# Performance work log

Hardware: AMD Instinct MI355X
Metric: run time of the kernel (lower is better)

Reference implementation:

```python
import jax, jax.numpy as jnp
import numpy as np

P = 8        # patch size
STRIDE = 4   # reference patch stride
SR = 12      # search radius
SS = 3       # search step -> 9x9 = 81 candidates
K = 16       # group size (3rd dim of 3D transform)
LAM = 2.7    # hard threshold multiplier
TWO_STEP = True


def _dct_mat(n):
    k = np.arange(n)[:, None].astype(np.float64)
    i = np.arange(n)[None, :].astype(np.float64)
    m = np.cos(np.pi * (2 * i + 1) * k / (2 * n)) * np.sqrt(2.0 / n)
    m[0] /= np.sqrt(2.0)
    return jnp.asarray(m, jnp.float32)


def _hadamard(n):
    h = np.array([[1.0]])
    while h.shape[0] < n:
        h = np.kron(h, np.array([[1.0, 1.0], [1.0, -1.0]])) / np.sqrt(2.0)
    return jnp.asarray(h, jnp.float32)

D8 = _dct_mat(P)
H16 = _hadamard(K)


def _extract_patches(img):
    # img (H, W) -> (Hp*Wp, P*P) patches at stride 1
    H, W = img.shape
    Hp, Wp = H - P + 1, W - P + 1
    cols = [img[di:di + Hp, dj:dj + Wp] for di in range(P) for dj in range(P)]
    return jnp.stack(cols, -1).reshape(Hp * Wp, P * P), Hp, Wp


def _block_match(patches, Hp, Wp):
    # returns (N, K) flat patch indices of best-matching groups
    ri = jnp.arange(0, Hp, STRIDE)
    rj = jnp.arange(0, Wp, STRIDE)
    RI, RJ = jnp.meshgrid(ri, rj, indexing='ij')
    RI, RJ = RI.reshape(-1), RJ.reshape(-1)                     # (N,)
    offs = jnp.arange(-SR, SR + 1, SS)
    OI, OJ = jnp.meshgrid(offs, offs, indexing='ij')
    ci = jnp.clip(RI[:, None] + OI.reshape(-1)[None, :], 0, Hp - 1)
    cj = jnp.clip(RJ[:, None] + OJ.reshape(-1)[None, :], 0, Wp - 1)
    cidx = ci * Wp + cj                                         # (N, C)
    cand = patches[cidx]                                        # (N, C, 64)
    ref = patches[RI * Wp + RJ]                                 # (N, 64)
    dist = (jnp.sum(cand * cand, -1)
            - 2.0 * jnp.einsum('nce,ne->nc', cand, ref)
            + jnp.sum(ref * ref, -1)[:, None])
    _, top = jax.lax.top_k(-dist, K)
    return jnp.take_along_axis(cidx, top, axis=1)               # (N, K)


def _fwd3d(groups):
    # (N, K, P*P) -> 3D transform coeffs (N, K, P, P)
    g = groups.reshape(groups.shape[0], K, P, P)
    c = jnp.einsum('ab,nkbc,dc->nkad', D8, g, D8)   # 2D DCT per patch
    return jnp.einsum('gk,nkad->ngad', H16, c)      # 1D Hadamard across group


def _inv3d(coef):
    c = jnp.einsum('gk,ngad->nkad', H16, coef)      # H^T (orthonormal)
    g = jnp.einsum('ab,nkad,dc->nkbc', D8, c, D8)   # inverse 2D DCT
    return g.reshape(coef.shape[0], K, P * P)


def _aggregate(vals, w, gidx, Hp, Wp, H, W):
    # vals (N,K,64) filtered patches, w (N,) group weights, gidx (N,K)
    gi, gj = gidx // Wp, gidx % Wp
    offs = (jnp.arange(P)[:, None] * W + jnp.arange(P)[None, :]).reshape(-1)
    pix = ((gi * W + gj)[..., None] + offs).reshape(-1)         # (N*K*64,)
    wv = jnp.broadcast_to(w[:, None, None], vals.shape)
    num = jnp.zeros(H * W, jnp.float32).at[pix].add((wv * vals).reshape(-1))
    den = jnp.zeros(H * W, jnp.float32).at[pix].add(wv.reshape(-1))
    return (num / jnp.maximum(den, 1e-8)).reshape(H, W)


def _bm3d_channel(img, sigma2):
    H, W = img.shape
    sigma2 = jnp.float32(sigma2)
    sigma = jnp.sqrt(sigma2)
    patches, Hp, Wp = _extract_patches(img)

    # ---- step 1: hard-threshold collaborative filtering ----
    gidx = _block_match(patches, Hp, Wp)
    groups = patches[gidx]                                      # (N,K,64)
    coef = _fwd3d(groups)
    mask = (jnp.abs(coef) > LAM * sigma)
    mask = mask.at[:, 0, 0, 0].set(True)                        # keep DC
    coef_ht = jnp.where(mask, coef, 0.0)
    nnz = jnp.sum(mask.astype(jnp.float32), axis=(1, 2, 3))
    w_ht = 1.0 / (sigma2 * jnp.maximum(nnz, 1.0))
    basic = _aggregate(_inv3d(coef_ht), w_ht, gidx, Hp, Wp, H, W)
    if not TWO_STEP:
        return basic

    # ---- step 2: Wiener filtering using the basic estimate ----
    patches_b, _, _ = _extract_patches(basic)
    gidx2 = _block_match(patches_b, Hp, Wp)
    cb = _fwd3d(patches_b[gidx2])                               # basic coeffs
    cn = _fwd3d(patches[gidx2])                                 # noisy coeffs
    wien = cb * cb / (cb * cb + sigma2)
    coef_w = wien * cn
    w_wie = 1.0 / (sigma2 * jnp.maximum(jnp.sum(wien * wien, axis=(1, 2, 3)), 1e-8))
    return _aggregate(_inv3d(coef_w), w_wie, gidx2, Hp, Wp, H, W)


def setup_inputs() -> dict:
    key = jax.random.key(0)
    im = jax.random.randint(key, (1, 1, 384, 384), 0, 256, dtype=jnp.int32)
    return {"im": im, "variance": 25}


def reference(im, variance):
    # im: (1, 1, H, W) int tensor, values >= 0; variance: scalar noise variance
    outs = [_bm3d_channel(im[0, c].astype(jnp.float32), variance)
            for c in range(im.shape[1])]
    return jnp.stack(outs, 0)[None]                             # (1, C, H, W) float32
```

## Files before the change

kernel.cpp:

```cpp
#include <hip/hip_runtime.h>
#include <math.h>

#define TS 45
#define FINF 3.4e38f

__device__ __forceinline__ int iclip(int v, int hi) {
  return v < 0 ? 0 : (v > hi ? hi : v);
}

constexpr float CA = 0.35355339059327373f;
constexpr float K1 = 0.49039264020161522f;
constexpr float K2 = 0.46193976625564337f;
constexpr float K3 = 0.41573480615127262f;
constexpr float K4 = 0.35355339059327379f;
constexpr float K5 = 0.27778511650980111f;
constexpr float K6 = 0.19134171618254489f;
constexpr float K7 = 0.097545161008064135f;

constexpr float DCT8[8][8] = {
  { CA, CA, CA, CA, CA, CA, CA, CA},
  { K1, K3, K5, K7,-K7,-K5,-K3,-K1},
  { K2, K6,-K6,-K2,-K2,-K6, K6, K2},
  { K3,-K7,-K1,-K5, K5, K1, K7,-K3},
  { K4,-K4,-K4, K4, K4,-K4,-K4, K4},
  { K5,-K1, K7, K3,-K3,-K7, K1,-K5},
  { K6,-K2, K2,-K6,-K6, K2,-K2, K6},
  { K7,-K5, K3,-K1, K1,-K3, K5,-K7},
};

__device__ __forceinline__ int sxor_i(int v, int m) {
  switch (m) {
    case 1:  return __builtin_amdgcn_update_dpp(0, v, 0xB1, 0xF, 0xF, true);
    case 2:  return __builtin_amdgcn_update_dpp(0, v, 0x4E, 0xF, 0xF, true);
    case 4:  return __builtin_amdgcn_ds_swizzle(v, (4 << 10) | 0x1F);
    case 8:  return __builtin_amdgcn_ds_swizzle(v, (8 << 10) | 0x1F);
    case 16: return __builtin_amdgcn_ds_swizzle(v, (16 << 10) | 0x1F);
    default: return __shfl_xor(v, 32, 64);
  }
}
__device__ __forceinline__ float sxor_f(float v, int m) {
  return __int_as_float(sxor_i(__float_as_int(v), m));
}

__device__ __forceinline__ float qbcast(float v, int s) {
  int x = __float_as_int(v), r;
  switch (s) {
    case 0:  r = __builtin_amdgcn_update_dpp(0, x, 0x00, 0xF, 0xF, true); break;
    case 1:  r = __builtin_amdgcn_update_dpp(0, x, 0x55, 0xF, 0xF, true); break;
    case 2:  r = __builtin_amdgcn_update_dpp(0, x, 0xAA, 0xF, 0xF, true); break;
    default: r = __builtin_amdgcn_update_dpp(0, x, 0xFF, 0xF, 0xF, true); break;
  }
  return __int_as_float(r);
}

__device__ __forceinline__ void fwd_rowcol(float X[2][8], float U[2][8],
                                           const float Ca0[8], const float Ca1[8]) {
#pragma unroll
  for (int r = 0; r < 2; r++)
#pragma unroll
    for (int d = 0; d < 8; d++) {
      float s = X[r][0] * DCT8[d][0];
#pragma unroll
      for (int c = 1; c < 8; c++) s += X[r][c] * DCT8[d][c];
      U[r][d] = s;
    }
#pragma unroll
  for (int r = 0; r < 2; r++)
#pragma unroll
    for (int d = 0; d < 8; d++) X[r][d] = 0.f;
#pragma unroll
  for (int b = 0; b < 8; b++)
#pragma unroll
    for (int d = 0; d < 8; d++) {
      float yb = qbcast(U[b & 1][d], b >> 1);
      X[0][d] += Ca0[b] * yb;
      X[1][d] += Ca1[b] * yb;
    }
}

__device__ __forceinline__ void inv_colrow(float X[2][8], float U[2][8],
                                           const float Ct0[8], const float Ct1[8]) {
#pragma unroll
  for (int r = 0; r < 2; r++)
#pragma unroll
    for (int d = 0; d < 8; d++) U[r][d] = 0.f;
#pragma unroll
  for (int a = 0; a < 8; a++)
#pragma unroll
    for (int d = 0; d < 8; d++) {
      float za = qbcast(X[a & 1][d], a >> 1);
      U[0][d] += Ct0[a] * za;
      U[1][d] += Ct1[a] * za;
    }
#pragma unroll
  for (int r = 0; r < 2; r++)
#pragma unroll
    for (int c = 0; c < 8; c++) {
      float s = U[r][0] * DCT8[0][c];
#pragma unroll
      for (int d = 1; d < 8; d++) s += U[r][d] * DCT8[d][c];
      X[r][c] = s;
    }
}

__device__ __forceinline__ void had16r(float X[2][8], int lane) {
#pragma unroll
  for (int m = 4; m <= 32; m <<= 1) {
    bool hi = (lane & m) != 0;
#pragma unroll
    for (int r = 0; r < 2; r++)
#pragma unroll
      for (int d = 0; d < 8; d++) {
        float tv = sxor_f(X[r][d], m);
        X[r][d] = hi ? (tv - X[r][d]) : (X[r][d] + tv);
      }
  }
#pragma unroll
  for (int r = 0; r < 2; r++)
#pragma unroll
    for (int d = 0; d < 8; d++) X[r][d] *= 0.25f;
}

template <int WIEN>
__device__ __forceinline__ void group_worker(
    const float* __restrict__ tileS, const float* __restrict__ tileN,
    float* __restrict__ accN, float* __restrict__ accD,
    const float* __restrict__ ldsD, int* __restrict__ sel,
    float* __restrict__ wdrow,
    int lane, int ri, int rj, int bi, int ub, float sigma2) {

  int cB = lane < 17 ? 64 + lane : 80;
  int aiA = iclip(ri + (lane / 9) * 3 - 12, 376) - bi;
  int ajA = iclip(rj + (lane % 9) * 3 - 12, 376) - ub;
  int aiB = iclip(ri + (cB / 9) * 3 - 12, 376) - bi;
  int ajB = iclip(rj + (cB % 9) * 3 - 12, 376) - ub;
  int roi = ri - bi, roj = rj - ub;
  float sccA = 0.f, scrA = 0.f, sccB = 0.f, scrB = 0.f, srr = 0.f;
#pragma unroll
  for (int i = 0; i < 8; i++) {
    const float* rr = tileS + (roi + i) * TS + roj;
    const float* ar = tileS + (aiA + i) * TS + ajA;
    const float* br = tileS + (aiB + i) * TS + ajB;
#pragma unroll
    for (int j = 0; j < 8; j++) {
      float rv = rr[j], av = ar[j], bv = br[j];
      sccA += av * av; scrA += av * rv;
      sccB += bv * bv; scrB += bv * rv;
      srr  += rv * rv;
    }
  }
  float d0 = sccA - 2.f * scrA + srr;
  float d1 = lane < 17 ? (sccB - 2.f * scrB + srr) : FINF;

  wdrow[lane] = d0;
  if (lane < 17)      wdrow[64 + lane] = d1;
  else if (lane < 20) wdrow[64 + lane] = FINF;

  int rank0 = 0, rank1 = 0;
  const float4* wp = (const float4*)wdrow;
  int idxB = 64 + lane;
#pragma unroll 3
  for (int c4 = 0; c4 < 21; c4++) {
    float4 v = wp[c4];
    float ev[4] = {v.x, v.y, v.z, v.w};
#pragma unroll
    for (int u = 0; u < 4; u++) {
      int c2 = c4 * 4 + u;
      rank0 += (ev[u] < d0 || (ev[u] == d0 && c2 < lane)) ? 1 : 0;
      rank1 += (ev[u] < d1 || (ev[u] == d1 && c2 < idxB)) ? 1 : 0;
    }
  }
  if (rank0 < 16) sel[rank0] = (aiA << 8) | ajA;
  if (lane < 17 && rank1 < 16) sel[rank1] = (aiB << 8) | ajB;

  int q = lane & 3, k = lane >> 2;
  float Ca0[8], Ca1[8];
#pragma unroll
  for (int b = 0; b < 8; b++) {
    Ca0[b] = ldsD[(2 * q) * 8 + b];
    Ca1[b] = ldsD[(2 * q + 1) * 8 + b];
  }
  int sp = sel[k];
  int gi = (sp >> 8) + 2 * q, gj = sp & 255;

  float X[2][8], U[2][8], ZB[2][8];
  float w;

  if (WIEN) {
#pragma unroll
    for (int r = 0; r < 2; r++)
#pragma unroll
      for (int c = 0; c < 8; c++) ZB[r][c] = tileS[(gi + r) * TS + gj + c];
    fwd_rowcol(ZB, U, Ca0, Ca1);
    had16r(ZB, lane);
  }

#pragma unroll
  for (int r = 0; r < 2; r++)
#pragma unroll
    for (int c = 0; c < 8; c++) X[r][c] = tileN[(gi + r) * TS + gj + c];
  fwd_rowcol(X, U, Ca0, Ca1);
  had16r(X, lane);

  if (WIEN) {
    float part = 0.f;
#pragma unroll
    for (int r = 0; r < 2; r++)
#pragma unroll
      for (int d = 0; d < 8; d++) {
        float cb = ZB[r][d];
        float we = cb * cb / (cb * cb + sigma2);
        X[r][d] = we * X[r][d];
        part += we * we;
      }
#pragma unroll
    for (int m = 1; m <= 32; m <<= 1) part += sxor_f(part, m);
    w = 1.f / (sigma2 * fmaxf(part, 1e-8f));
  } else {
    float thr = 2.7f * sqrtf(sigma2);
    int cnt = 0;
#pragma unroll
    for (int r = 0; r < 2; r++)
#pragma unroll
      for (int d = 0; d < 8; d++) {
        bool keep = (fabsf(X[r][d]) > thr) || (lane == 0 && r == 0 && d == 0);
        cnt += (int)__popcll(__ballot(keep));
        if (!keep) X[r][d] = 0.f;
      }
    w = 1.f / (sigma2 * fmaxf((float)cnt, 1.f));
  }

  had16r(X, lane);
#pragma unroll
  for (int a = 0; a < 8; a++) {
    Ca0[a] = ldsD[a * 8 + 2 * q];
    Ca1[a] = ldsD[a * 8 + 2 * q + 1];
  }
  inv_colrow(X, U, Ca0, Ca1);

#pragma unroll
  for (int r = 0; r < 2; r++)
#pragma unroll
    for (int c = 0; c < 8; c++) {
      int off = (gi + r) * TS + gj + c;
      atomicAdd(&accN[off], w * X[r][c]);
      atomicAdd(&accD[off], w);
    }
}

template <int WIEN>
__global__ __launch_bounds__(256, 6) void bm3d_pass(
    const int* __restrict__ img,
    const float* __restrict__ bn, const float* __restrict__ bd,
    const int* __restrict__ pvar,
    float* __restrict__ num, float* __restrict__ den) {
  __shared__ float ldsD[64];
  __shared__ int   ldsSel[4][16];
  __shared__ __align__(16) float wdist[4][84];
  __shared__ float tileN[32 * TS];
  __shared__ float tileB[WIEN ? 32 * TS : 1];
  __shared__ float accN[32 * TS], accD[32 * TS];

  int t = threadIdx.x;
  int brow = blockIdx.x / 24, bcb = blockIdx.x - brow * 24;
  int ri = brow * 4;
  int bim = ri - 12;      int bi = bim < 0 ? 0 : (bim > 352 ? 352 : bim);
  int ubm = 16 * bcb - 12; int ub = ubm < 0 ? 0 : (ubm > 352 ? 352 : ubm);

  if (t < 64) ldsD[t] = DCT8[t >> 3][t & 7];
  for (int e = t; e < 32 * 44; e += 256) {
    int r = e / 44, c = e - r * 44;
    int col = ub + c;
    bool ok = col < 384;
    int gidx = (bi + r) * 384 + col;
    tileN[r * TS + c] = ok ? (float)img[gidx] : 0.f;
    if (WIEN)
      tileB[r * TS + c] = ok ? (bn[gidx] / fmaxf(bd[gidx], 1e-8f)) : 0.f;
  }
  for (int e = t; e < 32 * TS; e += 256) { accN[e] = 0.f; accD[e] = 0.f; }
  __syncthreads();

  float sigma2 = (float)pvar[0];
  int wv = t >> 6, lane = t & 63;
  int gc = bcb * 4 + wv;
  if (gc < 95) {
    group_worker<WIEN>(WIEN ? tileB : tileN, tileN, accN, accD, ldsD,
                       &ldsSel[wv][0], &wdist[wv][0],
                       lane, ri, gc * 4, bi, ub, sigma2);
  }
  __syncthreads();

  for (int e = t; e < 32 * TS; e += 256) {
    float dv = accD[e];
    if (dv != 0.f) {
      int r = e / TS, c = e - r * TS;
      int gp = (bi + r) * 384 + ub + c;
      atomicAdd(&num[gp], accN[e]);
      atomicAdd(&den[gp], dv);
    }
  }
}

__global__ void div_kernel(const float* __restrict__ num,
                           const float* __restrict__ den,
                           float* __restrict__ out, int npix) {
  int i = blockIdx.x * blockDim.x + threadIdx.x;
  if (i < npix) out[i] = num[i] / fmaxf(den[i], 1e-8f);
}

extern "C" void kernel_launch(void* const* d_in, const int* in_sizes, int n_in,
                              void* d_out, int out_size, void* d_ws, size_t ws_size,
                              hipStream_t stream) {
  const int* img  = (const int*)d_in[0];
  const int* pvar = (const int*)d_in[1];
  float* out = (float*)d_out;
  float* ws  = (float*)d_ws;

  const int NPIX = 384 * 384;
  float* num1 = ws + 0 * NPIX;
  float* den1 = ws + 1 * NPIX;
  float* num2 = ws + 2 * NPIX;
  float* den2 = ws + 3 * NPIX;

  hipMemsetAsync(num1, 0, (size_t)4 * NPIX * sizeof(float), stream);

  const int NBLK = 95 * 24;
  bm3d_pass<0><<<NBLK, 256, 0, stream>>>(img, nullptr, nullptr, pvar, num1, den1);
  bm3d_pass<1><<<NBLK, 256, 0, stream>>>(img, num1, den1, pvar, num2, den2);
  div_kernel<<<(NPIX + 255) / 256, 256, 0, stream>>>(num2, den2, out, NPIX);
}
```

Before: 273.3 us.

## Replace global atomic aggregation with per-block slabs and a gather reduction

Each block now writes its local numerator and denominator tile to a private slab in workspace, where it previously did global atomicAdds. A separate reduce kernel gathers every overlapping block tile for each pixel and divides, producing the basic estimate and the final output. This removes the memset and the atomic contention, and folds the division for the basic estimate into the reduction. In exchange it writes about 26 MB of slab data per pass and needs enough workspace; otherwise it falls back to the atomic path.

```diff
diff --git a/kernel.cpp b/kernel.cpp
--- a/kernel.cpp
+++ b/kernel.cpp
@@ -3,6 +3,9 @@
 
 #define TS 45
 #define FINF 3.4e38f
+#define NPIX (384 * 384)
+#define NBLK (95 * 24)
+#define TILEPX (32 * 44)
 
 __device__ __forceinline__ int iclip(int v, int hi) {
   return v < 0 ? 0 : (v > hi ? hi : v);
@@ -248,7 +251,7 @@
     }
 }
 
-template <int WIEN>
+template <int WIEN, int SLAB>
 __global__ __launch_bounds__(256, 6) void bm3d_pass(
     const int* __restrict__ img,
     const float* __restrict__ bn, const float* __restrict__ bd,
@@ -274,8 +277,11 @@
     bool ok = col < 384;
     int gidx = (bi + r) * 384 + col;
     tileN[r * TS + c] = ok ? (float)img[gidx] : 0.f;
-    if (WIEN)
-      tileB[r * TS + c] = ok ? (bn[gidx] / fmaxf(bd[gidx], 1e-8f)) : 0.f;
+    if (WIEN) {
+      float bv = 0.f;
+      if (ok) bv = SLAB ? bn[gidx] : (bn[gidx] / fmaxf(bd[gidx], 1e-8f));
+      tileB[r * TS + c] = bv;
+    }
   }
   for (int e = t; e < 32 * TS; e += 256) { accN[e] = 0.f; accD[e] = 0.f; }
   __syncthreads();
@@ -290,15 +296,50 @@
   }
   __syncthreads();
 
-  for (int e = t; e < 32 * TS; e += 256) {
-    float dv = accD[e];
-    if (dv != 0.f) {
-      int r = e / TS, c = e - r * TS;
-      int gp = (bi + r) * 384 + ub + c;
-      atomicAdd(&num[gp], accN[e]);
-      atomicAdd(&den[gp], dv);
-    }
-  }
+  if (SLAB) {
+    float2* slab = (float2*)num + (size_t)blockIdx.x * TILEPX;
+    for (int e = t; e < TILEPX; e += 256) {
+      int r = e / 44, c = e - r * 44;
+      slab[e] = make_float2(accN[r * TS + c], accD[r * TS + c]);
+    }
+  } else {
+    for (int e = t; e < 32 * TS; e += 256) {
+      float dv = accD[e];
+      if (dv != 0.f) {
+        int r = e / TS, c = e - r * TS;
+        int gp = (bi + r) * 384 + ub + c;
+        atomicAdd(&num[gp], accN[e]);
+        atomicAdd(&den[gp], dv);
+      }
+    }
+  }
+}
+
+__global__ void reduce_kernel(const float2* __restrict__ slab,
+                              float* __restrict__ out) {
+  int p = blockIdx.x * blockDim.x + threadIdx.x;
+  if (p >= NPIX) return;
+  int y = p / 384, x = p - y * 384;
+
+  int rlo = (y - 31) / 4; if (rlo < 0) rlo = 0;
+  int rhi = ((y + 12) >> 2) + (y >= 352 ? 3 : 0); if (rhi > 94) rhi = 94;
+  int clo = (x - 31) / 16; if (clo < 0) clo = 0;
+  int chi = ((x + 12) >> 4) + (x >= 352 ? 1 : 0); if (chi > 23) chi = 23;
+
+  float n = 0.f, d = 0.f;
+  for (int br = rlo; br <= rhi; br++) {
+    int bim = br * 4 - 12; int bi = bim < 0 ? 0 : (bim > 352 ? 352 : bim);
+    int r = y - bi;
+    if (r < 0 || r >= 32) continue;
+    for (int bc = clo; bc <= chi; bc++) {
+      int ubm = 16 * bc - 12; int ub = ubm < 0 ? 0 : (ubm > 352 ? 352 : ubm);
+      int c = x - ub;
+      if (c < 0 || c >= 44) continue;
+      float2 v = slab[(size_t)(br * 24 + bc) * TILEPX + r * 44 + c];
+      n += v.x; d += v.y;
+    }
+  }
+  out[p] = n / fmaxf(d, 1e-8f);
 }
 
 __global__ void div_kernel(const float* __restrict__ num,
@@ -316,16 +357,28 @@
   float* out = (float*)d_out;
   float* ws  = (float*)d_ws;
 
-  const int NPIX = 384 * 384;
-  float* num1 = ws + 0 * NPIX;
-  float* den1 = ws + 1 * NPIX;
-  float* num2 = ws + 2 * NPIX;
-  float* den2 = ws + 3 * NPIX;
-
-  hipMemsetAsync(num1, 0, (size_t)4 * NPIX * sizeof(float), stream);
-
-  const int NBLK = 95 * 24;
-  bm3d_pass<0><<<NBLK, 256, 0, stream>>>(img, nullptr, nullptr, pvar, num1, den1);
-  bm3d_pass<1><<<NBLK, 256, 0, stream>>>(img, num1, den1, pvar, num2, den2);
-  div_kernel<<<(NPIX + 255) / 256, 256, 0, stream>>>(num2, den2, out, NPIX);
-}
+  const size_t slab_floats = (size_t)NBLK * TILEPX * 2;
+  const size_t need = (slab_floats + NPIX) * sizeof(float);
+
+  if (ws_size >= need) {
+    float2* slab = (float2*)ws;
+    float* basic = ws + slab_floats;
+    bm3d_pass<0, 1><<<NBLK, 256, 0, stream>>>(img, nullptr, nullptr, pvar,
+                                              (float*)slab, nullptr);
+    reduce_kernel<<<(NPIX + 255) / 256, 256, 0, stream>>>(slab, basic);
+    bm3d_pass<1, 1><<<NBLK, 256, 0, stream>>>(img, basic, nullptr, pvar,
+                                              (float*)slab, nullptr);
+    reduce_kernel<<<(NPIX + 255) / 256, 256, 0, stream>>>(slab, out);
+  } else {
+    float* num1 = ws + 0 * NPIX;
+    float* den1 = ws + 1 * NPIX;
+    float* num2 = ws + 2 * NPIX;
+    float* den2 = ws + 3 * NPIX;
+    hipMemsetAsync(num1, 0, (size_t)4 * NPIX * sizeof(float), stream);
+    bm3d_pass<0, 0><<<NBLK, 256, 0, stream>>>(img, nullptr, nullptr, pvar,
+                                              num1, den1);
+    bm3d_pass<1, 0><<<NBLK, 256, 0, stream>>>(img, num1, den1, pvar,
+                                              num2, den2);
+    div_kernel<<<(NPIX + 255) / 256, 256, 0, stream>>>(num2, den2, out, NPIX);
+  }
+}
```

Measured after the change: 309.3 us. 1.13x slower.

## Split each 3D group across two wavefronts with one patch row per lane

Applied to the files above, without the earlier changes.

Each group is now handled by two wavefronts (512 threads per block) instead of one. Each lane holds a single patch row rather than two, and the block-matching distance work is split by rows across the pair. The last Hadamard butterfly stage is exchanged through LDS between the paired waves, and the count or weight reduction also goes through LDS. The intent is to halve per-lane register and ALU work so more waves can be resident, at the cost of extra __syncthreads barriers and LDS traffic. It also swaps some cross-lane swizzles for DPP row broadcasts.

```diff
diff --git a/kernel.cpp b/kernel.cpp
--- a/kernel.cpp
+++ b/kernel.cpp
@@ -3,6 +3,7 @@
 
 #define TS 45
 #define FINF 3.4e38f
+#define NPIX (384 * 384)
 
 __device__ __forceinline__ int iclip(int v, int hi) {
   return v < 0 ? 0 : (v > hi ? hi : v);
@@ -33,7 +34,7 @@
     case 1:  return __builtin_amdgcn_update_dpp(0, v, 0xB1, 0xF, 0xF, true);
     case 2:  return __builtin_amdgcn_update_dpp(0, v, 0x4E, 0xF, 0xF, true);
     case 4:  return __builtin_amdgcn_ds_swizzle(v, (4 << 10) | 0x1F);
-    case 8:  return __builtin_amdgcn_ds_swizzle(v, (8 << 10) | 0x1F);
+    case 8:  return __builtin_amdgcn_update_dpp(0, v, 0x128, 0xF, 0xF, true);
     case 16: return __builtin_amdgcn_ds_swizzle(v, (16 << 10) | 0x1F);
     default: return __shfl_xor(v, 32, 64);
   }
@@ -42,221 +43,93 @@
   return __int_as_float(sxor_i(__float_as_int(v), m));
 }
 
-__device__ __forceinline__ float qbcast(float v, int s) {
+__device__ __forceinline__ float bcast8(float v, int b) {
   int x = __float_as_int(v), r;
-  switch (s) {
-    case 0:  r = __builtin_amdgcn_update_dpp(0, x, 0x00, 0xF, 0xF, true); break;
-    case 1:  r = __builtin_amdgcn_update_dpp(0, x, 0x55, 0xF, 0xF, true); break;
-    case 2:  r = __builtin_amdgcn_update_dpp(0, x, 0xAA, 0xF, 0xF, true); break;
-    default: r = __builtin_amdgcn_update_dpp(0, x, 0xFF, 0xF, 0xF, true); break;
+  switch (b) {
+    case 0: r = __builtin_amdgcn_ds_swizzle(x, (0 << 5) | 0x18); break;
+    case 1: r = __builtin_amdgcn_ds_swizzle(x, (1 << 5) | 0x18); break;
+    case 2: r = __builtin_amdgcn_ds_swizzle(x, (2 << 5) | 0x18); break;
+    case 3: r = __builtin_amdgcn_ds_swizzle(x, (3 << 5) | 0x18); break;
+    case 4: r = __builtin_amdgcn_ds_swizzle(x, (4 << 5) | 0x18); break;
+    case 5: r = __builtin_amdgcn_ds_swizzle(x, (5 << 5) | 0x18); break;
+    case 6: r = __builtin_amdgcn_ds_swizzle(x, (6 << 5) | 0x18); break;
+    default: r = __builtin_amdgcn_ds_swizzle(x, (7 << 5) | 0x18); break;
   }
   return __int_as_float(r);
 }
 
-__device__ __forceinline__ void fwd_rowcol(float X[2][8], float U[2][8],
-                                           const float Ca0[8], const float Ca1[8]) {
-#pragma unroll
-  for (int r = 0; r < 2; r++)
+__device__ __forceinline__ void fwd8(float X[8], const float Ca[8]) {
+  float U[8];
+#pragma unroll
+  for (int d = 0; d < 8; d++) {
+    float s = X[0] * DCT8[d][0];
+#pragma unroll
+    for (int c = 1; c < 8; c++) s += X[c] * DCT8[d][c];
+    U[d] = s;
+  }
+#pragma unroll
+  for (int d = 0; d < 8; d++) X[d] = 0.f;
+#pragma unroll
+  for (int b = 0; b < 8; b++)
+#pragma unroll
+    for (int d = 0; d < 8; d++) X[d] += Ca[b] * bcast8(U[d], b);
+}
+
+__device__ __forceinline__ void inv8(float X[8], const float Ct[8]) {
+  float U[8];
+#pragma unroll
+  for (int d = 0; d < 8; d++) U[d] = 0.f;
+#pragma unroll
+  for (int a = 0; a < 8; a++)
+#pragma unroll
+    for (int d = 0; d < 8; d++) U[d] += Ct[a] * bcast8(X[d], a);
+#pragma unroll
+  for (int c = 0; c < 8; c++) {
+    float s = U[0] * DCT8[0][c];
+#pragma unroll
+    for (int d = 1; d < 8; d++) s += U[d] * DCT8[d][c];
+    X[c] = s;
+  }
+}
+
+__device__ __forceinline__ void had16x(float X[8], int lane, int gwave,
+                                       float4* xs, const float4* xp) {
+#pragma unroll
+  for (int m = 8; m <= 32; m <<= 1) {
+    bool hi = (lane & m) != 0;
 #pragma unroll
     for (int d = 0; d < 8; d++) {
-      float s = X[r][0] * DCT8[d][0];
-#pragma unroll
-      for (int c = 1; c < 8; c++) s += X[r][c] * DCT8[d][c];
-      U[r][d] = s;
-    }
-#pragma unroll
-  for (int r = 0; r < 2; r++)
-#pragma unroll
-    for (int d = 0; d < 8; d++) X[r][d] = 0.f;
-#pragma unroll
-  for (int b = 0; b < 8; b++)
-#pragma unroll
-    for (int d = 0; d < 8; d++) {
-      float yb = qbcast(U[b & 1][d], b >> 1);
-      X[0][d] += Ca0[b] * yb;
-      X[1][d] += Ca1[b] * yb;
-    }
-}
-
-__device__ __forceinline__ void inv_colrow(float X[2][8], float U[2][8],
-                                           const float Ct0[8], const float Ct1[8]) {
-#pragma unroll
-  for (int r = 0; r < 2; r++)
-#pragma unroll
-    for (int d = 0; d < 8; d++) U[r][d] = 0.f;
-#pragma unroll
-  for (int a = 0; a < 8; a++)
-#pragma unroll
-    for (int d = 0; d < 8; d++) {
-      float za = qbcast(X[a & 1][d], a >> 1);
-      U[0][d] += Ct0[a] * za;
-      U[1][d] += Ct1[a] * za;
-    }
-#pragma unroll
-  for (int r = 0; r < 2; r++)
-#pragma unroll
-    for (int c = 0; c < 8; c++) {
-      float s = U[r][0] * DCT8[0][c];
-#pragma unroll
-      for (int d = 1; d < 8; d++) s += U[r][d] * DCT8[d][c];
-      X[r][c] = s;
-    }
-}
-
-__device__ __forceinline__ void had16r(float X[2][8], int lane) {
-#pragma unroll
-  for (int m = 4; m <= 32; m <<= 1) {
-    bool hi = (lane & m) != 0;
-#pragma unroll
-    for (int r = 0; r < 2; r++)
-#pragma unroll
-      for (int d = 0; d < 8; d++) {
-        float tv = sxor_f(X[r][d], m);
-        X[r][d] = hi ? (tv - X[r][d]) : (X[r][d] + tv);
-      }
-  }
-#pragma unroll
-  for (int r = 0; r < 2; r++)
-#pragma unroll
-    for (int d = 0; d < 8; d++) X[r][d] *= 0.25f;
+      float tv = sxor_f(X[d], m);
+      X[d] = hi ? (tv - X[d]) : (X[d] + tv);
+    }
+  }
+  bool hi = gwave != 0;
+#pragma unroll
+  for (int d0 = 0; d0 < 8; d0 += 4) {
+    *xs = make_float4(X[d0], X[d0 + 1], X[d0 + 2], X[d0 + 3]);
+    __syncthreads();
+    float4 tv = *xp;
+    X[d0]     = hi ? (tv.x - X[d0])     : (X[d0] + tv.x);
+    X[d0 + 1] = hi ? (tv.y - X[d0 + 1]) : (X[d0 + 1] + tv.y);
+    X[d0 + 2] = hi ? (tv.z - X[d0 + 2]) : (X[d0 + 2] + tv.z);
+    X[d0 + 3] = hi ? (tv.w - X[d0 + 3]) : (X[d0 + 3] + tv.w);
+    __syncthreads();
+  }
+#pragma unroll
+  for (int d = 0; d < 8; d++) X[d] *= 0.25f;
 }
 
 template <int WIEN>
-__device__ __forceinline__ void group_worker(
-    const float* __restrict__ tileS, const float* __restrict__ tileN,
-    float* __restrict__ accN, float* __restrict__ accD,
-    const float* __restrict__ ldsD, int* __restrict__ sel,
-    float* __restrict__ wdrow,
-    int lane, int ri, int rj, int bi, int ub, float sigma2) {
-
-  int cB = lane < 17 ? 64 + lane : 80;
-  int aiA = iclip(ri + (lane / 9) * 3 - 12, 376) - bi;
-  int ajA = iclip(rj + (lane % 9) * 3 - 12, 376) - ub;
-  int aiB = iclip(ri + (cB / 9) * 3 - 12, 376) - bi;
-  int ajB = iclip(rj + (cB % 9) * 3 - 12, 376) - ub;
-  int roi = ri - bi, roj = rj - ub;
-  float sccA = 0.f, scrA = 0.f, sccB = 0.f, scrB = 0.f, srr = 0.f;
-#pragma unroll
-  for (int i = 0; i < 8; i++) {
-    const float* rr = tileS + (roi + i) * TS + roj;
-    const float* ar = tileS + (aiA + i) * TS + ajA;
-    const float* br = tileS + (aiB + i) * TS + ajB;
-#pragma unroll
-    for (int j = 0; j < 8; j++) {
-      float rv = rr[j], av = ar[j], bv = br[j];
-      sccA += av * av; scrA += av * rv;
-      sccB += bv * bv; scrB += bv * rv;
-      srr  += rv * rv;
-    }
-  }
-  float d0 = sccA - 2.f * scrA + srr;
-  float d1 = lane < 17 ? (sccB - 2.f * scrB + srr) : FINF;
-
-  wdrow[lane] = d0;
-  if (lane < 17)      wdrow[64 + lane] = d1;
-  else if (lane < 20) wdrow[64 + lane] = FINF;
-
-  int rank0 = 0, rank1 = 0;
-  const float4* wp = (const float4*)wdrow;
-  int idxB = 64 + lane;
-#pragma unroll 3
-  for (int c4 = 0; c4 < 21; c4++) {
-    float4 v = wp[c4];
-    float ev[4] = {v.x, v.y, v.z, v.w};
-#pragma unroll
-    for (int u = 0; u < 4; u++) {
-      int c2 = c4 * 4 + u;
-      rank0 += (ev[u] < d0 || (ev[u] == d0 && c2 < lane)) ? 1 : 0;
-      rank1 += (ev[u] < d1 || (ev[u] == d1 && c2 < idxB)) ? 1 : 0;
-    }
-  }
-  if (rank0 < 16) sel[rank0] = (aiA << 8) | ajA;
-  if (lane < 17 && rank1 < 16) sel[rank1] = (aiB << 8) | ajB;
-
-  int q = lane & 3, k = lane >> 2;
-  float Ca0[8], Ca1[8];
-#pragma unroll
-  for (int b = 0; b < 8; b++) {
-    Ca0[b] = ldsD[(2 * q) * 8 + b];
-    Ca1[b] = ldsD[(2 * q + 1) * 8 + b];
-  }
-  int sp = sel[k];
-  int gi = (sp >> 8) + 2 * q, gj = sp & 255;
-
-  float X[2][8], U[2][8], ZB[2][8];
-  float w;
-
-  if (WIEN) {
-#pragma unroll
-    for (int r = 0; r < 2; r++)
-#pragma unroll
-      for (int c = 0; c < 8; c++) ZB[r][c] = tileS[(gi + r) * TS + gj + c];
-    fwd_rowcol(ZB, U, Ca0, Ca1);
-    had16r(ZB, lane);
-  }
-
-#pragma unroll
-  for (int r = 0; r < 2; r++)
-#pragma unroll
-    for (int c = 0; c < 8; c++) X[r][c] = tileN[(gi + r) * TS + gj + c];
-  fwd_rowcol(X, U, Ca0, Ca1);
-  had16r(X, lane);
-
-  if (WIEN) {
-    float part = 0.f;
-#pragma unroll
-    for (int r = 0; r < 2; r++)
-#pragma unroll
-      for (int d = 0; d < 8; d++) {
-        float cb = ZB[r][d];
-        float we = cb * cb / (cb * cb + sigma2);
-        X[r][d] = we * X[r][d];
-        part += we * we;
-      }
-#pragma unroll
-    for (int m = 1; m <= 32; m <<= 1) part += sxor_f(part, m);
-    w = 1.f / (sigma2 * fmaxf(part, 1e-8f));
-  } else {
-    float thr = 2.7f * sqrtf(sigma2);
-    int cnt = 0;
-#pragma unroll
-    for (int r = 0; r < 2; r++)
-#pragma unroll
-      for (int d = 0; d < 8; d++) {
-        bool keep = (fabsf(X[r][d]) > thr) || (lane == 0 && r == 0 && d == 0);
-        cnt += (int)__popcll(__ballot(keep));
-        if (!keep) X[r][d] = 0.f;
-      }
-    w = 1.f / (sigma2 * fmaxf((float)cnt, 1.f));
-  }
-
-  had16r(X, lane);
-#pragma unroll
-  for (int a = 0; a < 8; a++) {
-    Ca0[a] = ldsD[a * 8 + 2 * q];
-    Ca1[a] = ldsD[a * 8 + 2 * q + 1];
-  }
-  inv_colrow(X, U, Ca0, Ca1);
-
-#pragma unroll
-  for (int r = 0; r < 2; r++)
-#pragma unroll
-    for (int c = 0; c < 8; c++) {
-      int off = (gi + r) * TS + gj + c;
-      atomicAdd(&accN[off], w * X[r][c]);
-      atomicAdd(&accD[off], w);
-    }
-}
-
-template <int WIEN>
-__global__ __launch_bounds__(256, 6) void bm3d_pass(
+__global__ __launch_bounds__(512, 8) void bm3d_pass(
     const int* __restrict__ img,
     const float* __restrict__ bn, const float* __restrict__ bd,
     const int* __restrict__ pvar,
     float* __restrict__ num, float* __restrict__ den) {
   __shared__ float ldsD[64];
-  __shared__ int   ldsSel[4][16];
-  __shared__ __align__(16) float wdist[4][84];
+  __shared__ int   wsel[4][16];
+  __shared__ __align__(16) float wdistP[8][84];
+  __shared__ float4 xbuf[8][64];
+  __shared__ float pbuf[8];
   __shared__ float tileN[32 * TS];
   __shared__ float tileB[WIEN ? 32 * TS : 1];
   __shared__ float accN[32 * TS], accD[32 * TS];
@@ -264,11 +137,11 @@
   int t = threadIdx.x;
   int brow = blockIdx.x / 24, bcb = blockIdx.x - brow * 24;
   int ri = brow * 4;
-  int bim = ri - 12;      int bi = bim < 0 ? 0 : (bim > 352 ? 352 : bim);
+  int bim = ri - 12;       int bi = bim < 0 ? 0 : (bim > 352 ? 352 : bim);
   int ubm = 16 * bcb - 12; int ub = ubm < 0 ? 0 : (ubm > 352 ? 352 : ubm);
 
   if (t < 64) ldsD[t] = DCT8[t >> 3][t & 7];
-  for (int e = t; e < 32 * 44; e += 256) {
+  for (int e = t; e < 32 * 44; e += 512) {
     int r = e / 44, c = e - r * 44;
     int col = ub + c;
     bool ok = col < 384;
@@ -277,20 +150,151 @@
     if (WIEN)
       tileB[r * TS + c] = ok ? (bn[gidx] / fmaxf(bd[gidx], 1e-8f)) : 0.f;
   }
-  for (int e = t; e < 32 * TS; e += 256) { accN[e] = 0.f; accD[e] = 0.f; }
+  for (int e = t; e < 32 * TS; e += 512) { accN[e] = 0.f; accD[e] = 0.f; }
   __syncthreads();
 
   float sigma2 = (float)pvar[0];
   int wv = t >> 6, lane = t & 63;
-  int gc = bcb * 4 + wv;
-  if (gc < 95) {
-    group_worker<WIEN>(WIEN ? tileB : tileN, tileN, accN, accD, ldsD,
-                       &ldsSel[wv][0], &wdist[wv][0],
-                       lane, ri, gc * 4, bi, ub, sigma2);
-  }
+  int gl = wv >> 1, gwave = wv & 1;
+  int gc = bcb * 4 + gl;
+  bool active = gc < 95;
+  int rj = (active ? gc : 94) * 4;
+  const float* tileS = WIEN ? tileB : tileN;
+
+  int cB = lane < 17 ? 64 + lane : 80;
+  int aiA = iclip(ri + (lane / 9) * 3 - 12, 376) - bi;
+  int ajA = iclip(rj + (lane % 9) * 3 - 12, 376) - ub;
+  int aiB = iclip(ri + (cB / 9) * 3 - 12, 376) - bi;
+  int ajB = iclip(rj + (cB % 9) * 3 - 12, 376) - ub;
+  int roi = ri - bi, roj = rj - ub;
+  int r0 = gwave * 4;
+  float sccA = 0.f, scrA = 0.f, sccB = 0.f, scrB = 0.f, srr = 0.f;
+#pragma unroll
+  for (int i = 0; i < 4; i++) {
+    int row = r0 + i;
+    const float* rr = tileS + (roi + row) * TS + roj;
+    const float* ar = tileS + (aiA + row) * TS + ajA;
+    const float* br = tileS + (aiB + row) * TS + ajB;
+#pragma unroll
+    for (int j = 0; j < 8; j++) {
+      float rv = rr[j], av = ar[j], bv = br[j];
+      sccA += av * av; scrA += av * rv;
+      sccB += bv * bv; scrB += bv * rv;
+      srr  += rv * rv;
+    }
+  }
+  float dAp = sccA - 2.f * scrA + srr;
+  float dBp = sccB - 2.f * scrB + srr;
+  wdistP[wv][lane] = dAp;
+  if (lane < 17)      wdistP[wv][64 + lane] = dBp;
+  else if (lane < 20) wdistP[wv][64 + lane] = gwave ? 0.f : FINF;
   __syncthreads();
 
-  for (int e = t; e < 32 * TS; e += 256) {
+  float dme; int idxme, smine;
+  if (gwave == 0) {
+    dme = wdistP[2 * gl][lane] + wdistP[2 * gl + 1][lane];
+    idxme = lane; smine = (aiA << 8) | ajA;
+  } else {
+    dme = lane < 17 ? (wdistP[2 * gl][64 + lane] + wdistP[2 * gl + 1][64 + lane])
+                    : FINF;
+    idxme = 64 + lane; smine = (aiB << 8) | ajB;
+  }
+  {
+    int rank = 0;
+    const float4* p0 = (const float4*)&wdistP[2 * gl][0];
+    const float4* p1 = (const float4*)&wdistP[2 * gl + 1][0];
+#pragma unroll 3
+    for (int c4 = 0; c4 < 21; c4++) {
+      float4 v = p0[c4], u = p1[c4];
+      float ev[4] = {v.x + u.x, v.y + u.y, v.z + u.z, v.w + u.w};
+#pragma unroll
+      for (int j = 0; j < 4; j++) {
+        int c2 = c4 * 4 + j;
+        rank += (ev[j] < dme || (ev[j] == dme && c2 < idxme)) ? 1 : 0;
+      }
+    }
+    bool dowrite = (gwave == 0) || (lane < 17);
+    if (dowrite && rank < 16) wsel[gl][rank] = smine;
+  }
+  __syncthreads();
+
+  int k = (gwave << 3) | (lane >> 3);
+  int r8 = lane & 7;
+  int sp = wsel[gl][k];
+  int gi = (sp >> 8) + r8, gj = sp & 255;
+
+  float Ca[8];
+  *(float4*)&Ca[0] = *(const float4*)&ldsD[r8 * 8];
+  *(float4*)&Ca[4] = *(const float4*)&ldsD[r8 * 8 + 4];
+
+  float4* xs = &xbuf[wv][lane];
+  const float4* xp = &xbuf[wv ^ 1][lane];
+
+  float X[8], w;
+
+  if (WIEN) {
+    float Z[8];
+#pragma unroll
+    for (int c = 0; c < 8; c++) Z[c] = tileS[gi * TS + gj + c];
+    fwd8(Z, Ca);
+    had16x(Z, lane, gwave, xs, xp);
+
+#pragma unroll
+    for (int c = 0; c < 8; c++) X[c] = tileN[gi * TS + gj + c];
+    fwd8(X, Ca);
+    had16x(X, lane, gwave, xs, xp);
+
+    float part = 0.f;
+#pragma unroll
+    for (int d = 0; d < 8; d++) {
+      float cb = Z[d];
+      float we = cb * cb / (cb * cb + sigma2);
+      X[d] = we * X[d];
+      part += we * we;
+    }
+#pragma unroll
+    for (int m = 1; m <= 32; m <<= 1) part += sxor_f(part, m);
+    if (lane == 0) pbuf[wv] = part;
+    __syncthreads();
+    float tot = pbuf[2 * gl] + pbuf[2 * gl + 1];
+    w = 1.f / (sigma2 * fmaxf(tot, 1e-8f));
+  } else {
+#pragma unroll
+    for (int c = 0; c < 8; c++) X[c] = tileN[gi * TS + gj + c];
+    fwd8(X, Ca);
+    had16x(X, lane, gwave, xs, xp);
+
+    float thr = 2.7f * sqrtf(sigma2);
+    int cnt = 0;
+#pragma unroll
+    for (int d = 0; d < 8; d++) {
+      bool keep = (fabsf(X[d]) > thr) || (gwave == 0 && lane == 0 && d == 0);
+      cnt += (int)__popcll(__ballot(keep));
+      if (!keep) X[d] = 0.f;
+    }
+    if (lane == 0) pbuf[wv] = (float)cnt;
+    __syncthreads();
+    float tot = pbuf[2 * gl] + pbuf[2 * gl + 1];
+    w = 1.f / (sigma2 * fmaxf(tot, 1.f));
+  }
+
+  had16x(X, lane, gwave, xs, xp);
+  float Ct[8];
+#pragma unroll
+  for (int a = 0; a < 8; a++) Ct[a] = ldsD[a * 8 + r8];
+  inv8(X, Ct);
+
+  if (active) {
+#pragma unroll
+    for (int c = 0; c < 8; c++) {
+      int off = gi * TS + gj + c;
+      atomicAdd(&accN[off], w * X[c]);
+      atomicAdd(&accD[off], w);
+    }
+  }
+  __syncthreads();
+
+  for (int e = t; e < 32 * TS; e += 512) {
     float dv = accD[e];
     if (dv != 0.f) {
       int r = e / TS, c = e - r * TS;
@@ -316,7 +320,6 @@
   float* out = (float*)d_out;
   float* ws  = (float*)d_ws;
 
-  const int NPIX = 384 * 384;
   float* num1 = ws + 0 * NPIX;
   float* den1 = ws + 1 * NPIX;
   float* num2 = ws + 2 * NPIX;
@@ -325,7 +328,7 @@
   hipMemsetAsync(num1, 0, (size_t)4 * NPIX * sizeof(float), stream);
 
   const int NBLK = 95 * 24;
-  bm3d_pass<0><<<NBLK, 256, 0, stream>>>(img, nullptr, nullptr, pvar, num1, den1);
-  bm3d_pass<1><<<NBLK, 256, 0, stream>>>(img, num1, den1, pvar, num2, den2);
+  bm3d_pass<0><<<NBLK, 512, 0, stream>>>(img, nullptr, nullptr, pvar, num1, den1);
+  bm3d_pass<1><<<NBLK, 512, 0, stream>>>(img, num1, den1, pvar, num2, den2);
   div_kernel<<<(NPIX + 255) / 256, 256, 0, stream>>>(num2, den2, out, NPIX);
 }
```

Result: slower. 306.7 us (+12.2%).
